# Kernel optimization log

Hardware: AMD Instinct MI355X
Metric: run time of the kernel (lower is better)

The kernel has to match this reference:

```python
import jax, jax.numpy as jnp
import numpy as np

B, S, F = 1024, 256, 64
HD = 64          # hidden_size
MEM = 10         # attention_memory
TIME_IDX = 0


def setup_inputs() -> dict:
    key = jax.random.key(0)
    ks = jax.random.split(key, 20)
    sc = 0.05
    d = {}
    d["x"] = jax.random.normal(ks[0], (B, S, F), dtype=jnp.float32)
    # layer 0 cell: linear_s in = HD+F+1; gates (f,i,T,u,o) stacked: in = HD+F+HD, out = 5*HD
    d["Ws0"] = jax.random.normal(ks[1], (HD + F + 1, HD), dtype=jnp.float32) * sc
    d["bs0"] = jnp.zeros((HD,), dtype=jnp.float32)
    d["Wg0"] = jax.random.normal(ks[2], (HD + F + HD, 5 * HD), dtype=jnp.float32) * sc
    d["bg0"] = jnp.zeros((5 * HD,), dtype=jnp.float32)
    # layer 1 cell: input is h of layer 0 (HD wide)
    d["Ws1"] = jax.random.normal(ks[3], (HD + HD + 1, HD), dtype=jnp.float32) * sc
    d["bs1"] = jnp.zeros((HD,), dtype=jnp.float32)
    d["Wg1"] = jax.random.normal(ks[4], (HD + HD + HD, 5 * HD), dtype=jnp.float32) * sc
    d["bg1"] = jnp.zeros((5 * HD,), dtype=jnp.float32)
    # attention params
    d["Waq"] = jax.random.normal(ks[5], (2 * HD, HD), dtype=jnp.float32) * sc
    d["baq"] = jnp.zeros((HD,), dtype=jnp.float32)
    d["Wah"] = jax.random.normal(ks[6], (HD, HD), dtype=jnp.float32) * sc
    d["bah"] = jnp.zeros((HD,), dtype=jnp.float32)
    d["bias_a"] = jnp.zeros((HD,), dtype=jnp.float32)
    d["v"] = jnp.ones((HD,), dtype=jnp.float32)
    d["Wint"] = jax.random.normal(ks[7], (2 * HD, HD), dtype=jnp.float32) * sc
    d["bint"] = jnp.zeros((HD,), dtype=jnp.float32)
    return d


def _cell(x_t, d_t, h, c, Ws, bs, Wg, bg):
    # s_t = tanh(linear_s([h, x, delta]))
    s = jnp.tanh(jnp.concatenate([h, x_t, d_t], axis=1) @ Ws + bs)
    # fused gate projection: [f, i, T, u(zeta), o] on [h, x, s]
    g = jnp.concatenate([h, x_t, s], axis=1) @ Wg + bg
    f, i, T, u, o = jnp.split(g, 5, axis=1)
    f = jax.nn.sigmoid(f)
    i = jax.nn.sigmoid(i)
    T = jax.nn.sigmoid(T)
    u = jnp.tanh(u)
    o = jax.nn.sigmoid(o)
    c_new = f * c + i * u + T * s
    h_new = o * jnp.tanh(c_new)
    return h_new, c_new


def reference(x, Ws0, bs0, Wg0, bg0, Ws1, bs1, Wg1, bg1,
              Waq, baq, Wah, bah, bias_a, v, Wint, bint):
    b, s_len, _ = x.shape
    hd = bs0.shape[0]
    # delta_t = time[t] - time[t-1], zero at t=0  -> [B, S, 1]
    time = x[:, :, TIME_IDX]
    delta = jnp.concatenate(
        [jnp.zeros((b, 1), dtype=x.dtype), time[:, 1:] - time[:, :-1]], axis=1)[:, :, None]

    xs = jnp.moveaxis(x, 1, 0)       # [S, B, F]
    ds = jnp.moveaxis(delta, 1, 0)   # [S, B, 1]

    def step(carry, inp):
        h0, c0, h1, c1 = carry
        x_t, d_t = inp
        h0, c0 = _cell(x_t, d_t, h0, c0, Ws0, bs0, Wg0, bg0)
        h1, c1 = _cell(h0, d_t, h1, c1, Ws1, bs1, Wg1, bg1)
        return (h0, c0, h1, c1), h1

    z = jnp.zeros((b, hd), dtype=x.dtype)
    (h0, c0, h1, c1), Hseq = jax.lax.scan(step, (z, z, z, z), (xs, ds))
    H = jnp.moveaxis(Hseq, 0, 1)     # [B, S, HD]

    mem = min(s_len, MEM)
    H_mem = H[:, s_len - mem:, :]    # [B, mem, HD]

    q_proj = jnp.concatenate([h1, c1], axis=1) @ Waq + baq   # [B, HD]
    H_proj = H_mem @ Wah + bah                                # [B, mem, HD]
    scores = jnp.tanh(q_proj[:, None, :] + H_proj + bias_a) @ v  # [B, mem]
    alpha = jax.nn.softmax(scores, axis=1)
    e_t = jnp.einsum('bm,bmh->bh', alpha, H_mem)
    final_repr = jnp.tanh(jnp.concatenate([h1, e_t], axis=1) @ Wint + bint)
    return final_repr
```

## Files before the change

kernel.cpp:

```cpp
#include <hip/hip_runtime.h>
#include <math.h>

#define HD    64
#define SLEN  256
#define BATCH 1024
#define TBB   16
#define NB    (BATCH / TBB)
#define NT    256
#define MEMN  10

typedef short bf16x8 __attribute__((ext_vector_type(8)));
typedef float f32x4  __attribute__((ext_vector_type(4)));
typedef unsigned short u16x4 __attribute__((ext_vector_type(4)));

#define MFMA16(a, b, c) __builtin_amdgcn_mfma_f32_16x16x32_bf16((a), (b), (c), 0, 0, 0)

#define OFF_WGL 122880
#define OFF_WSH 245760
#define OFF_WSL 262144
#define OFF_WSR_BYTES 557056

__device__ __forceinline__ unsigned short f2bf(float f) {
  unsigned u = __float_as_uint(f);
  u += 0x7fffu + ((u >> 16) & 1u);
  return (unsigned short)(u >> 16);
}
__device__ __forceinline__ float bf2f(unsigned short h) {
  return __uint_as_float(((unsigned)h) << 16);
}

__device__ __forceinline__ float frcp(float x) {
#if __has_builtin(__builtin_amdgcn_rcpf)
  return __builtin_amdgcn_rcpf(x);
#else
  return 1.0f / x;
#endif
}
__device__ __forceinline__ float fsigm(float v) { return frcp(1.0f + __expf(-v)); }
__device__ __forceinline__ float ftanh(float v) { return 2.0f * frcp(1.0f + __expf(-2.0f * v)) - 1.0f; }

__device__ __forceinline__ void bar_lds() {
  asm volatile("s_waitcnt lgkmcnt(0)" ::: "memory");
  __builtin_amdgcn_s_barrier();
  asm volatile("" ::: "memory");
}

__global__ void __launch_bounds__(256)
prep_pack(const float* __restrict__ Wg0, const float* __restrict__ Wg1,
          const float* __restrict__ Ws0, const float* __restrict__ Ws1,
          unsigned short* __restrict__ ws)
{
  const int idx = blockIdx.x * 256 + threadIdx.x;
  const int NWG = 2 * 20 * 6 * 64 * 8;
  const int NWS = 2 * 4 * 4 * 64 * 8;
  if (idx < NWG) {
    int L = idx / 61440, r0 = idx % 61440;
    int tile = r0 / 3072, r1 = r0 % 3072;
    int ks = r1 / 512, r2 = r1 % 512;
    int lane = r2 / 8, j = r2 % 8;
    int row = ks * 32 + (lane >> 4) * 8 + j;
    int col = tile * 16 + (lane & 15);
    float v = (L ? Wg1 : Wg0)[row * 320 + col];
    unsigned short h = f2bf(v);
    ws[idx] = h;
    ws[OFF_WGL + idx] = f2bf(v - bf2f(h));
  } else if (idx < NWG + NWS) {
    int k = idx - NWG;
    int L = k / 8192, r0 = k % 8192;
    int tile = r0 / 2048, r1 = r0 % 2048;
    int ks = r1 / 512, r2 = r1 % 512;
    int lane = r2 / 8, j = r2 % 8;
    int row = ks * 32 + (lane >> 4) * 8 + j;
    int col = tile * 16 + (lane & 15);
    float v = (L ? Ws1 : Ws0)[row * 64 + col];
    unsigned short h = f2bf(v);
    ws[OFF_WSH + k] = h;
    ws[OFF_WSL + k] = f2bf(v - bf2f(h));
  } else if (idx < NWG + NWS + 128) {
    int k = idx - NWG - NWS;
    int L = k / 64, c = k % 64;
    float* wsr = (float*)((char*)ws + OFF_WSR_BYTES);
    wsr[k] = (L ? Ws1 : Ws0)[128 * 64 + c];
  }
}

struct __align__(16) Smem {
  unsigned short XbH[2][16][216];
  unsigned short XbL[2][16][216];
  unsigned short WgC[2][5][4][2][512];
  float Hm[MEMN][16][64];
  float dlt[2][16];
  float h1s[16][68];
  float c1s[16][68];
};

__global__ void __launch_bounds__(NT, 1)
thlstm_mfma(const float* __restrict__ x, const unsigned short* __restrict__ wpack,
            const float* __restrict__ bs0, const float* __restrict__ bg0,
            const float* __restrict__ bs1, const float* __restrict__ bg1,
            const float* __restrict__ Waq, const float* __restrict__ gbaq,
            const float* __restrict__ Wah, const float* __restrict__ gbah,
            const float* __restrict__ gba,  const float* __restrict__ gv,
            const float* __restrict__ Wint, const float* __restrict__ gbint,
            float* __restrict__ out)
{
  __shared__ Smem sm;
  const int tid = threadIdx.x;
  const int w = tid >> 6, l = tid & 63;
  const int lg = l >> 4, lr = l & 15;
  const int c = w * 16 + lr;
  const int b0 = blockIdx.x * TBB;
  const int xrow = tid >> 4, xq = tid & 15;

  const unsigned short* WgH = wpack;
  const unsigned short* WgL = wpack + OFF_WGL;
  const unsigned short* WsH = wpack + OFF_WSH;
  const unsigned short* WsL = wpack + OFF_WSL;
  const float* WsR = (const float*)((const char*)wpack + OFF_WSR_BYTES);

  for (int i = tid; i < 2 * 16 * 216; i += NT) {
    ((unsigned short*)sm.XbH)[i] = 0;
    ((unsigned short*)sm.XbL)[i] = 0;
  }
  for (int i = tid; i < 5120; i += NT) {
    const int chunk = i & 63, frag = i >> 6;
    const int p = frag & 1, tt = (frag >> 1) & 3;
    const int g = (frag >> 3) % 5, L = (frag >> 3) / 5;
    const unsigned short* src = (p ? WgL : WgH) + ((L * 20 + g * 4 + tt) * 6 + 0) * 512 + chunk * 8;
    *(bf16x8*)&sm.WgC[L][g][tt][p][chunk * 8] = *(const bf16x8*)src;
  }
  if (xq == 0) { sm.dlt[0][xrow] = 0.f; sm.dlt[1][xrow] = 0.f; }

  bf16x8 wsW[2][4][2];
  bf16x8 wgT[2][5][2][2];
#pragma unroll
  for (int L = 0; L < 2; ++L) {
#pragma unroll
    for (int ks = 0; ks < 4; ++ks) {
      const int o = ((L * 4 + w) * 4 + ks) * 512 + l * 8;
      wsW[L][ks][0] = *(const bf16x8*)(WsH + o);
      wsW[L][ks][1] = *(const bf16x8*)(WsL + o);
    }
#pragma unroll
    for (int g = 0; g < 5; ++g)
#pragma unroll
      for (int k2 = 0; k2 < 2; ++k2) {
        const int o = ((L * 20 + g * 4 + w) * 6 + 4 + k2) * 512 + l * 8;
        wgT[L][g][k2][0] = *(const bf16x8*)(WgH + o);
        wgT[L][g][k2][1] = *(const bf16x8*)(WgL + o);
      }
  }
  float bsr[2]  = { bs0[c], bs1[c] };
  float wsrr[2] = { WsR[c], WsR[64 + c] };
  float bgr[2][5];
#pragma unroll
  for (int g = 0; g < 5; ++g) { bgr[0][g] = bg0[g * 64 + c]; bgr[1][g] = bg1[g * 64 + c]; }

  f32x4 xreg = *(const f32x4*)&x[((size_t)(b0 + xrow) * SLEN + 0) * HD + xq * 4];
  float prev0 = xreg[0];
  {
    u16x4 ph, pl;
#pragma unroll
    for (int k = 0; k < 4; ++k) {
      unsigned short hh = f2bf(xreg[k]);
      ph[k] = hh; pl[k] = f2bf(xreg[k] - bf2f(hh));
    }
    *(u16x4*)&sm.XbH[0][xrow][64 + xq * 4] = ph;
    *(u16x4*)&sm.XbL[0][xrow][64 + xq * 4] = pl;
  }
  bar_lds();
  xreg = *(const f32x4*)&x[((size_t)(b0 + xrow) * SLEN + 1) * HD + xq * 4];

  float cst[2][4] = {{0.f,0.f,0.f,0.f},{0.f,0.f,0.f,0.f}};
  float h1v[4] = {0.f,0.f,0.f,0.f};

  bf16x8 w1H[5], w1L[5];
#pragma unroll
  for (int g = 0; g < 5; ++g) {
    const int o1 = ((0 * 20 + g * 4 + w) * 6 + 1) * 512 + l * 8;
    w1H[g] = *(const bf16x8*)(WgH + o1);
    w1L[g] = *(const bf16x8*)(WgL + o1);
  }

  for (int t = 0; t < SLEN; ++t) {
#pragma unroll
    for (int L = 0; L < 2; ++L) {
      bf16x8 w2H[5], w2L[5], w3H[5], w3L[5];
#pragma unroll
      for (int g = 0; g < 5; ++g) {
        const int o2 = ((L * 20 + g * 4 + w) * 6 + 2) * 512 + l * 8;
        const int o3 = ((L * 20 + g * 4 + w) * 6 + 3) * 512 + l * 8;
        w2H[g] = *(const bf16x8*)(WgH + o2);
        w2L[g] = *(const bf16x8*)(WgL + o2);
        w3H[g] = *(const bf16x8*)(WgH + o3);
        w3L[g] = *(const bf16x8*)(WgL + o3);
      }
      bf16x8 aH[4], aL[4];
#pragma unroll
      for (int ks = 0; ks < 4; ++ks) {
        aH[ks] = *(const bf16x8*)&sm.XbH[L][lr][ks * 32 + lg * 8];
        aL[ks] = *(const bf16x8*)&sm.XbL[L][lr][ks * 32 + lg * 8];
      }
      f32x4 sHH = {0.f,0.f,0.f,0.f}, sHL = {0.f,0.f,0.f,0.f}, sLH = {0.f,0.f,0.f,0.f};
#pragma unroll
      for (int ks = 0; ks < 4; ++ks) {
        sHH = MFMA16(aH[ks], wsW[L][ks][0], sHH);
        sHL = MFMA16(aH[ks], wsW[L][ks][1], sHL);
        sLH = MFMA16(aL[ks], wsW[L][ks][0], sLH);
      }
      f32x4 gacc[5];
#pragma unroll
      for (int g = 0; g < 5; ++g) {
        bf16x8 cH = *(const bf16x8*)&sm.WgC[L][g][w][0][l * 8];
        bf16x8 cL = *(const bf16x8*)&sm.WgC[L][g][w][1][l * 8];
        f32x4 acc = {0.f,0.f,0.f,0.f};
        acc = MFMA16(aH[0], cH, acc);
        acc = MFMA16(aH[0], cL, acc);
        acc = MFMA16(aL[0], cH, acc);
        gacc[g] = acc;
      }
#pragma unroll
      for (int g = 0; g < 5; ++g) {
        gacc[g] = MFMA16(aH[1], w1H[g], gacc[g]);
        gacc[g] = MFMA16(aH[1], w1L[g], gacc[g]);
        gacc[g] = MFMA16(aL[1], w1H[g], gacc[g]);
      }
      f32x4 sacc = (sHH + sHL) + sLH;
      float sv[4];
      const float* dltc = sm.dlt[t & 1];
#pragma unroll
      for (int q = 0; q < 4; ++q) {
        const int r = lg * 4 + q;
        sv[q] = ftanh(sacc[q] + bsr[L] + dltc[r] * wsrr[L]);
        unsigned short hh = f2bf(sv[q]);
        sm.XbH[L][r][128 + c] = hh;
        sm.XbL[L][r][128 + c] = f2bf(sv[q] - bf2f(hh));
      }
#pragma unroll
      for (int g = 0; g < 5; ++g) {
        gacc[g] = MFMA16(aH[2], w2H[g], gacc[g]);
        gacc[g] = MFMA16(aH[2], w2L[g], gacc[g]);
        gacc[g] = MFMA16(aL[2], w2H[g], gacc[g]);
      }
      bar_lds();

      bf16x8 sHf[2], sLf[2];
#pragma unroll
      for (int k2 = 0; k2 < 2; ++k2) {
        sHf[k2] = *(const bf16x8*)&sm.XbH[L][lr][128 + k2 * 32 + lg * 8];
        sLf[k2] = *(const bf16x8*)&sm.XbL[L][lr][128 + k2 * 32 + lg * 8];
      }
#pragma unroll
      for (int g = 0; g < 5; ++g) {
        gacc[g] = MFMA16(aH[3], w3H[g], gacc[g]);
        gacc[g] = MFMA16(aH[3], w3L[g], gacc[g]);
        gacc[g] = MFMA16(aL[3], w3H[g], gacc[g]);
      }
#pragma unroll
      for (int k2 = 0; k2 < 2; ++k2)
#pragma unroll
        for (int g = 0; g < 5; ++g) {
          gacc[g] = MFMA16(sHf[k2], wgT[L][g][k2][0], gacc[g]);
          gacc[g] = MFMA16(sHf[k2], wgT[L][g][k2][1], gacc[g]);
          gacc[g] = MFMA16(sLf[k2], wgT[L][g][k2][0], gacc[g]);
        }
      {
        const int nL = 1 - L;
#pragma unroll
        for (int g = 0; g < 5; ++g) {
          const int o1 = ((nL * 20 + g * 4 + w) * 6 + 1) * 512 + l * 8;
          w1H[g] = *(const bf16x8*)(WgH + o1);
          w1L[g] = *(const bf16x8*)(WgL + o1);
        }
      }
#pragma unroll
      for (int q = 0; q < 4; ++q) {
        const int r = lg * 4 + q;
        const float fg = fsigm(gacc[0][q] + bgr[L][0]);
        const float ig = fsigm(gacc[1][q] + bgr[L][1]);
        const float Tg = fsigm(gacc[2][q] + bgr[L][2]);
        const float ug = ftanh(gacc[3][q] + bgr[L][3]);
        const float og = fsigm(gacc[4][q] + bgr[L][4]);
        const float cn = fg * cst[L][q] + ig * ug + Tg * sv[q];
        cst[L][q] = cn;
        const float hn = og * ftanh(cn);
        const unsigned short hh = f2bf(hn), hl = f2bf(hn - bf2f(hh));
        if (L == 0) {
          sm.XbH[0][r][c] = hh;      sm.XbL[0][r][c] = hl;
          sm.XbH[1][r][64 + c] = hh; sm.XbL[1][r][64 + c] = hl;
        } else {
          sm.XbH[1][r][c] = hh;      sm.XbL[1][r][c] = hl;
          h1v[q] = hn;
          if (t >= SLEN - MEMN) sm.Hm[t - (SLEN - MEMN)][r][c] = hn;
        }
      }
      if (L == 0) {
        if (xq == 0) { sm.dlt[(t + 1) & 1][xrow] = xreg[0] - prev0; prev0 = xreg[0]; }
        u16x4 ph, pl;
#pragma unroll
        for (int k = 0; k < 4; ++k) {
          unsigned short hh = f2bf(xreg[k]);
          ph[k] = hh; pl[k] = f2bf(xreg[k] - bf2f(hh));
        }
        *(u16x4*)&sm.XbH[0][xrow][64 + xq * 4] = ph;
        *(u16x4*)&sm.XbL[0][xrow][64 + xq * 4] = pl;
        const int tn = (t + 2 < SLEN) ? (t + 2) : (SLEN - 1);
        xreg = *(const f32x4*)&x[((size_t)(b0 + xrow) * SLEN + tn) * HD + xq * 4];
      }
      bar_lds();
    }
  }

#pragma unroll
  for (int q = 0; q < 4; ++q) {
    const int r = lg * 4 + q;
    sm.h1s[r][c] = h1v[q];
    sm.c1s[r][c] = cst[1][q];
  }
  bar_lds();

  float evs[4];
#pragma unroll
  for (int ri = 0; ri < 4; ++ri) {
    const int r = 4 * w + ri;
    const int j = l;
    float qv = gbaq[j];
    for (int k = 0; k < 64; ++k) qv += sm.h1s[r][k] * Waq[k * 64 + j];
    for (int k = 0; k < 64; ++k) qv += sm.c1s[r][k] * Waq[(64 + k) * 64 + j];
    float sc[MEMN];
#pragma unroll
    for (int m = 0; m < MEMN; ++m) {
      float hp = gbah[j];
      for (int k = 0; k < 64; ++k) hp += sm.Hm[m][r][k] * Wah[k * 64 + j];
      float tv = tanhf(qv + hp + gba[j]) * gv[j];
#pragma unroll
      for (int off = 32; off; off >>= 1) tv += __shfl_xor(tv, off, 64);
      sc[m] = tv;
    }
    float mx = sc[0];
#pragma unroll
    for (int m = 1; m < MEMN; ++m) mx = fmaxf(mx, sc[m]);
    float den = 0.f;
#pragma unroll
    for (int m = 0; m < MEMN; ++m) { sc[m] = expf(sc[m] - mx); den += sc[m]; }
    const float inv = 1.f / den;
    float ev = 0.f;
#pragma unroll
    for (int m = 0; m < MEMN; ++m) ev += sc[m] * sm.Hm[m][r][j];
    evs[ri] = ev * inv;
  }
  float (*es)[68] = sm.c1s;
#pragma unroll
  for (int ri = 0; ri < 4; ++ri) es[4 * w + ri][l] = evs[ri];
  bar_lds();
#pragma unroll
  for (int ri = 0; ri < 4; ++ri) {
    const int r = 4 * w + ri;
    const int j = l;
    float acc = gbint[j];
    for (int k = 0; k < 64; ++k) acc += sm.h1s[r][k] * Wint[k * 64 + j];
    for (int k = 0; k < 64; ++k) acc += es[r][k] * Wint[(64 + k) * 64 + j];
    out[(size_t)(b0 + r) * HD + j] = tanhf(acc);
  }
}

extern "C" void kernel_launch(void* const* d_in, const int* in_sizes, int n_in,
                              void* d_out, int out_size, void* d_ws, size_t ws_size,
                              hipStream_t stream) {
  const float* x      = (const float*)d_in[0];
  const float* Ws0    = (const float*)d_in[1];
  const float* bs0    = (const float*)d_in[2];
  const float* Wg0    = (const float*)d_in[3];
  const float* bg0    = (const float*)d_in[4];
  const float* Ws1    = (const float*)d_in[5];
  const float* bs1    = (const float*)d_in[6];
  const float* Wg1    = (const float*)d_in[7];
  const float* bg1    = (const float*)d_in[8];
  const float* Waq    = (const float*)d_in[9];
  const float* baq    = (const float*)d_in[10];
  const float* Wah    = (const float*)d_in[11];
  const float* bah    = (const float*)d_in[12];
  const float* bias_a = (const float*)d_in[13];
  const float* v      = (const float*)d_in[14];
  const float* Wint   = (const float*)d_in[15];
  const float* bint   = (const float*)d_in[16];
  float* out = (float*)d_out;

  const int total = 2 * 20 * 6 * 64 * 8 + 2 * 4 * 4 * 64 * 8 + 128;
  prep_pack<<<(total + 255) / 256, 256, 0, stream>>>(Wg0, Wg1, Ws0, Ws1,
                                                     (unsigned short*)d_ws);
  thlstm_mfma<<<NB, NT, 0, stream>>>(x, (const unsigned short*)d_ws,
                                     bs0, bg0, bs1, bg1,
                                     Waq, baq, Wah, bah, bias_a, v, Wint, bint, out);
}
```

Baseline: 1.279 ms.

## Skew two LSTM layers into wavefront so both run per tick

Restructures the recurrence so that each tick computes layer 0 at time t and layer 1 at time t-1 together, with a prologue for layer 0 at t=0 and an epilogue for layer 1 at the last step. This halves the number of barrier-separated phases per timestep and exposes two independent MFMA chains to interleave, hiding latency. In exchange, register pressure roughly doubles (two sets of weight fragments and accumulators), which may lower occupancy or cause spills, and the code grows.

```diff
diff --git a/kernel.cpp b/kernel.cpp
--- a/kernel.cpp
+++ b/kernel.cpp
@@ -8,6 +8,7 @@
 #define NB    (BATCH / TBB)
 #define NT    256
 #define MEMN  10
+#define LASTT (SLEN - MEMN)
 
 typedef short bf16x8 __attribute__((ext_vector_type(8)));
 typedef float f32x4  __attribute__((ext_vector_type(4)));
@@ -174,140 +175,385 @@
   float cst[2][4] = {{0.f,0.f,0.f,0.f},{0.f,0.f,0.f,0.f}};
   float h1v[4] = {0.f,0.f,0.f,0.f};
 
-  bf16x8 w1H[5], w1L[5];
-#pragma unroll
-  for (int g = 0; g < 5; ++g) {
-    const int o1 = ((0 * 20 + g * 4 + w) * 6 + 1) * 512 + l * 8;
-    w1H[g] = *(const bf16x8*)(WgH + o1);
-    w1L[g] = *(const bf16x8*)(WgL + o1);
-  }
-
-  for (int t = 0; t < SLEN; ++t) {
-#pragma unroll
-    for (int L = 0; L < 2; ++L) {
-      bf16x8 w2H[5], w2L[5], w3H[5], w3L[5];
-#pragma unroll
-      for (int g = 0; g < 5; ++g) {
-        const int o2 = ((L * 20 + g * 4 + w) * 6 + 2) * 512 + l * 8;
-        const int o3 = ((L * 20 + g * 4 + w) * 6 + 3) * 512 + l * 8;
-        w2H[g] = *(const bf16x8*)(WgH + o2);
-        w2L[g] = *(const bf16x8*)(WgL + o2);
-        w3H[g] = *(const bf16x8*)(WgH + o3);
-        w3L[g] = *(const bf16x8*)(WgL + o3);
-      }
-      bf16x8 aH[4], aL[4];
+  {
+    bf16x8 w1H[5], w1L[5];
+#pragma unroll
+    for (int g = 0; g < 5; ++g) {
+      const int o1 = ((g * 4 + w) * 6 + 1) * 512 + l * 8;
+      w1H[g] = *(const bf16x8*)(WgH + o1);
+      w1L[g] = *(const bf16x8*)(WgL + o1);
+    }
+    bf16x8 aH[4], aL[4];
+#pragma unroll
+    for (int ks = 0; ks < 4; ++ks) {
+      aH[ks] = *(const bf16x8*)&sm.XbH[0][lr][ks * 32 + lg * 8];
+      aL[ks] = *(const bf16x8*)&sm.XbL[0][lr][ks * 32 + lg * 8];
+    }
+    f32x4 sHH = {0,0,0,0}, sHL = {0,0,0,0}, sLH = {0,0,0,0};
+#pragma unroll
+    for (int ks = 0; ks < 4; ++ks) {
+      sHH = MFMA16(aH[ks], wsW[0][ks][0], sHH);
+      sHL = MFMA16(aH[ks], wsW[0][ks][1], sHL);
+      sLH = MFMA16(aL[ks], wsW[0][ks][0], sLH);
+    }
+    f32x4 gacc[5];
+#pragma unroll
+    for (int g = 0; g < 5; ++g) {
+      bf16x8 cH = *(const bf16x8*)&sm.WgC[0][g][w][0][l * 8];
+      bf16x8 cL = *(const bf16x8*)&sm.WgC[0][g][w][1][l * 8];
+      f32x4 acc = {0,0,0,0};
+      acc = MFMA16(aH[0], cH, acc);
+      acc = MFMA16(aH[0], cL, acc);
+      acc = MFMA16(aL[0], cH, acc);
+      gacc[g] = acc;
+    }
+    bf16x8 w2H[5], w2L[5];
+#pragma unroll
+    for (int g = 0; g < 5; ++g) {
+      const int o2 = ((g * 4 + w) * 6 + 2) * 512 + l * 8;
+      w2H[g] = *(const bf16x8*)(WgH + o2);
+      w2L[g] = *(const bf16x8*)(WgL + o2);
+      gacc[g] = MFMA16(aH[1], w1H[g], gacc[g]);
+      gacc[g] = MFMA16(aH[1], w1L[g], gacc[g]);
+      gacc[g] = MFMA16(aL[1], w1H[g], gacc[g]);
+    }
+    f32x4 sacc = (sHH + sHL) + sLH;
+    float sv[4];
+#pragma unroll
+    for (int q = 0; q < 4; ++q) {
+      const int r = lg * 4 + q;
+      sv[q] = ftanh(sacc[q] + bsr[0]);
+      unsigned short hh = f2bf(sv[q]);
+      sm.XbH[0][r][128 + c] = hh;
+      sm.XbL[0][r][128 + c] = f2bf(sv[q] - bf2f(hh));
+    }
+#pragma unroll
+    for (int g = 0; g < 5; ++g) {
+      gacc[g] = MFMA16(aH[2], w2H[g], gacc[g]);
+      gacc[g] = MFMA16(aH[2], w2L[g], gacc[g]);
+      gacc[g] = MFMA16(aL[2], w2H[g], gacc[g]);
+    }
+    bar_lds();
+    bf16x8 w3H[5], w3L[5];
+#pragma unroll
+    for (int g = 0; g < 5; ++g) {
+      const int o3 = ((g * 4 + w) * 6 + 3) * 512 + l * 8;
+      w3H[g] = *(const bf16x8*)(WgH + o3);
+      w3L[g] = *(const bf16x8*)(WgL + o3);
+    }
+    bf16x8 sHf[2], sLf[2];
+#pragma unroll
+    for (int k2 = 0; k2 < 2; ++k2) {
+      sHf[k2] = *(const bf16x8*)&sm.XbH[0][lr][128 + k2 * 32 + lg * 8];
+      sLf[k2] = *(const bf16x8*)&sm.XbL[0][lr][128 + k2 * 32 + lg * 8];
+    }
+#pragma unroll
+    for (int k2 = 0; k2 < 2; ++k2)
+#pragma unroll
+      for (int g = 0; g < 5; ++g) {
+        gacc[g] = MFMA16(sHf[k2], wgT[0][g][k2][0], gacc[g]);
+        gacc[g] = MFMA16(sHf[k2], wgT[0][g][k2][1], gacc[g]);
+        gacc[g] = MFMA16(sLf[k2], wgT[0][g][k2][0], gacc[g]);
+      }
+#pragma unroll
+    for (int g = 0; g < 5; ++g) {
+      gacc[g] = MFMA16(aH[3], w3H[g], gacc[g]);
+      gacc[g] = MFMA16(aH[3], w3L[g], gacc[g]);
+      gacc[g] = MFMA16(aL[3], w3H[g], gacc[g]);
+    }
+#pragma unroll
+    for (int q = 0; q < 4; ++q) {
+      const int r = lg * 4 + q;
+      const float fg = fsigm(gacc[0][q] + bgr[0][0]);
+      const float ig = fsigm(gacc[1][q] + bgr[0][1]);
+      const float Tg = fsigm(gacc[2][q] + bgr[0][2]);
+      const float ug = ftanh(gacc[3][q] + bgr[0][3]);
+      const float og = fsigm(gacc[4][q] + bgr[0][4]);
+      const float cn = fg * cst[0][q] + ig * ug + Tg * sv[q];
+      cst[0][q] = cn;
+      const float hn = og * ftanh(cn);
+      const unsigned short hh = f2bf(hn), hl = f2bf(hn - bf2f(hh));
+      sm.XbH[0][r][c] = hh;      sm.XbL[0][r][c] = hl;
+      sm.XbH[1][r][64 + c] = hh; sm.XbL[1][r][64 + c] = hl;
+    }
+    if (xq == 0) { sm.dlt[1][xrow] = xreg[0] - prev0; prev0 = xreg[0]; }
+    {
+      u16x4 ph, pl;
+#pragma unroll
+      for (int k = 0; k < 4; ++k) {
+        unsigned short hh = f2bf(xreg[k]);
+        ph[k] = hh; pl[k] = f2bf(xreg[k] - bf2f(hh));
+      }
+      *(u16x4*)&sm.XbH[0][xrow][64 + xq * 4] = ph;
+      *(u16x4*)&sm.XbL[0][xrow][64 + xq * 4] = pl;
+    }
+    xreg = *(const f32x4*)&x[((size_t)(b0 + xrow) * SLEN + 2) * HD + xq * 4];
+    bar_lds();
+  }
+
+  for (int tick = 1; tick < SLEN; ++tick) {
+    bf16x8 w1H[2][5], w1L[2][5];
+#pragma unroll
+    for (int Lc = 0; Lc < 2; ++Lc)
+#pragma unroll
+      for (int g = 0; g < 5; ++g) {
+        const int o1 = ((Lc * 20 + g * 4 + w) * 6 + 1) * 512 + l * 8;
+        w1H[Lc][g] = *(const bf16x8*)(WgH + o1);
+        w1L[Lc][g] = *(const bf16x8*)(WgL + o1);
+      }
+    bf16x8 aH[2][4], aL[2][4];
+#pragma unroll
+    for (int Lc = 0; Lc < 2; ++Lc)
 #pragma unroll
       for (int ks = 0; ks < 4; ++ks) {
-        aH[ks] = *(const bf16x8*)&sm.XbH[L][lr][ks * 32 + lg * 8];
-        aL[ks] = *(const bf16x8*)&sm.XbL[L][lr][ks * 32 + lg * 8];
-      }
-      f32x4 sHH = {0.f,0.f,0.f,0.f}, sHL = {0.f,0.f,0.f,0.f}, sLH = {0.f,0.f,0.f,0.f};
+        aH[Lc][ks] = *(const bf16x8*)&sm.XbH[Lc][lr][ks * 32 + lg * 8];
+        aL[Lc][ks] = *(const bf16x8*)&sm.XbL[Lc][lr][ks * 32 + lg * 8];
+      }
+    f32x4 sHH[2], sHL[2], sLH[2];
+#pragma unroll
+    for (int Lc = 0; Lc < 2; ++Lc) {
+      sHH[Lc] = (f32x4){0,0,0,0}; sHL[Lc] = (f32x4){0,0,0,0}; sLH[Lc] = (f32x4){0,0,0,0};
 #pragma unroll
       for (int ks = 0; ks < 4; ++ks) {
-        sHH = MFMA16(aH[ks], wsW[L][ks][0], sHH);
-        sHL = MFMA16(aH[ks], wsW[L][ks][1], sHL);
-        sLH = MFMA16(aL[ks], wsW[L][ks][0], sLH);
-      }
-      f32x4 gacc[5];
-#pragma unroll
-      for (int g = 0; g < 5; ++g) {
-        bf16x8 cH = *(const bf16x8*)&sm.WgC[L][g][w][0][l * 8];
-        bf16x8 cL = *(const bf16x8*)&sm.WgC[L][g][w][1][l * 8];
-        f32x4 acc = {0.f,0.f,0.f,0.f};
-        acc = MFMA16(aH[0], cH, acc);
-        acc = MFMA16(aH[0], cL, acc);
-        acc = MFMA16(aL[0], cH, acc);
-        gacc[g] = acc;
-      }
-#pragma unroll
-      for (int g = 0; g < 5; ++g) {
-        gacc[g] = MFMA16(aH[1], w1H[g], gacc[g]);
-        gacc[g] = MFMA16(aH[1], w1L[g], gacc[g]);
-        gacc[g] = MFMA16(aL[1], w1H[g], gacc[g]);
-      }
-      f32x4 sacc = (sHH + sHL) + sLH;
-      float sv[4];
-      const float* dltc = sm.dlt[t & 1];
+        sHH[Lc] = MFMA16(aH[Lc][ks], wsW[Lc][ks][0], sHH[Lc]);
+        sHL[Lc] = MFMA16(aH[Lc][ks], wsW[Lc][ks][1], sHL[Lc]);
+        sLH[Lc] = MFMA16(aL[Lc][ks], wsW[Lc][ks][0], sLH[Lc]);
+      }
+    }
+    f32x4 gacc[2][5];
+#pragma unroll
+    for (int Lc = 0; Lc < 2; ++Lc)
+#pragma unroll
+      for (int g = 0; g < 5; ++g) {
+        bf16x8 cH = *(const bf16x8*)&sm.WgC[Lc][g][w][0][l * 8];
+        bf16x8 cL = *(const bf16x8*)&sm.WgC[Lc][g][w][1][l * 8];
+        f32x4 acc = {0,0,0,0};
+        acc = MFMA16(aH[Lc][0], cH, acc);
+        acc = MFMA16(aH[Lc][0], cL, acc);
+        acc = MFMA16(aL[Lc][0], cH, acc);
+        gacc[Lc][g] = acc;
+      }
+    bf16x8 w2H[2][5], w2L[2][5];
+#pragma unroll
+    for (int Lc = 0; Lc < 2; ++Lc)
+#pragma unroll
+      for (int g = 0; g < 5; ++g) {
+        const int o2 = ((Lc * 20 + g * 4 + w) * 6 + 2) * 512 + l * 8;
+        w2H[Lc][g] = *(const bf16x8*)(WgH + o2);
+        w2L[Lc][g] = *(const bf16x8*)(WgL + o2);
+        gacc[Lc][g] = MFMA16(aH[Lc][1], w1H[Lc][g], gacc[Lc][g]);
+        gacc[Lc][g] = MFMA16(aH[Lc][1], w1L[Lc][g], gacc[Lc][g]);
+        gacc[Lc][g] = MFMA16(aL[Lc][1], w1H[Lc][g], gacc[Lc][g]);
+      }
+    float sv[2][4];
+    const float* dltA = sm.dlt[tick & 1];
+    const float* dltB = sm.dlt[(tick & 1) ^ 1];
+#pragma unroll
+    for (int Lc = 0; Lc < 2; ++Lc) {
+      const float* dltc = Lc ? dltB : dltA;
+      f32x4 sacc = (sHH[Lc] + sHL[Lc]) + sLH[Lc];
 #pragma unroll
       for (int q = 0; q < 4; ++q) {
         const int r = lg * 4 + q;
-        sv[q] = ftanh(sacc[q] + bsr[L] + dltc[r] * wsrr[L]);
-        unsigned short hh = f2bf(sv[q]);
-        sm.XbH[L][r][128 + c] = hh;
-        sm.XbL[L][r][128 + c] = f2bf(sv[q] - bf2f(hh));
-      }
-#pragma unroll
-      for (int g = 0; g < 5; ++g) {
-        gacc[g] = MFMA16(aH[2], w2H[g], gacc[g]);
-        gacc[g] = MFMA16(aH[2], w2L[g], gacc[g]);
-        gacc[g] = MFMA16(aL[2], w2H[g], gacc[g]);
-      }
-      bar_lds();
-
-      bf16x8 sHf[2], sLf[2];
+        sv[Lc][q] = ftanh(sacc[q] + bsr[Lc] + dltc[r] * wsrr[Lc]);
+        unsigned short hh = f2bf(sv[Lc][q]);
+        sm.XbH[Lc][r][128 + c] = hh;
+        sm.XbL[Lc][r][128 + c] = f2bf(sv[Lc][q] - bf2f(hh));
+      }
+    }
+#pragma unroll
+    for (int Lc = 0; Lc < 2; ++Lc)
+#pragma unroll
+      for (int g = 0; g < 5; ++g) {
+        gacc[Lc][g] = MFMA16(aH[Lc][2], w2H[Lc][g], gacc[Lc][g]);
+        gacc[Lc][g] = MFMA16(aH[Lc][2], w2L[Lc][g], gacc[Lc][g]);
+        gacc[Lc][g] = MFMA16(aL[Lc][2], w2H[Lc][g], gacc[Lc][g]);
+      }
+    bar_lds();
+
+    bf16x8 w3H[2][5], w3L[2][5];
+#pragma unroll
+    for (int Lc = 0; Lc < 2; ++Lc)
+#pragma unroll
+      for (int g = 0; g < 5; ++g) {
+        const int o3 = ((Lc * 20 + g * 4 + w) * 6 + 3) * 512 + l * 8;
+        w3H[Lc][g] = *(const bf16x8*)(WgH + o3);
+        w3L[Lc][g] = *(const bf16x8*)(WgL + o3);
+      }
+    bf16x8 sHf[2][2], sLf[2][2];
+#pragma unroll
+    for (int Lc = 0; Lc < 2; ++Lc)
 #pragma unroll
       for (int k2 = 0; k2 < 2; ++k2) {
-        sHf[k2] = *(const bf16x8*)&sm.XbH[L][lr][128 + k2 * 32 + lg * 8];
-        sLf[k2] = *(const bf16x8*)&sm.XbL[L][lr][128 + k2 * 32 + lg * 8];
-      }
-#pragma unroll
-      for (int g = 0; g < 5; ++g) {
-        gacc[g] = MFMA16(aH[3], w3H[g], gacc[g]);
-        gacc[g] = MFMA16(aH[3], w3L[g], gacc[g]);
-        gacc[g] = MFMA16(aL[3], w3H[g], gacc[g]);
-      }
+        sHf[Lc][k2] = *(const bf16x8*)&sm.XbH[Lc][lr][128 + k2 * 32 + lg * 8];
+        sLf[Lc][k2] = *(const bf16x8*)&sm.XbL[Lc][lr][128 + k2 * 32 + lg * 8];
+      }
+#pragma unroll
+    for (int Lc = 0; Lc < 2; ++Lc)
 #pragma unroll
       for (int k2 = 0; k2 < 2; ++k2)
 #pragma unroll
         for (int g = 0; g < 5; ++g) {
-          gacc[g] = MFMA16(sHf[k2], wgT[L][g][k2][0], gacc[g]);
-          gacc[g] = MFMA16(sHf[k2], wgT[L][g][k2][1], gacc[g]);
-          gacc[g] = MFMA16(sLf[k2], wgT[L][g][k2][0], gacc[g]);
+          gacc[Lc][g] = MFMA16(sHf[Lc][k2], wgT[Lc][g][k2][0], gacc[Lc][g]);
+          gacc[Lc][g] = MFMA16(sHf[Lc][k2], wgT[Lc][g][k2][1], gacc[Lc][g]);
+          gacc[Lc][g] = MFMA16(sLf[Lc][k2], wgT[Lc][g][k2][0], gacc[Lc][g]);
         }
+#pragma unroll
+    for (int Lc = 0; Lc < 2; ++Lc)
+#pragma unroll
+      for (int g = 0; g < 5; ++g) {
+        gacc[Lc][g] = MFMA16(aH[Lc][3], w3H[Lc][g], gacc[Lc][g]);
+        gacc[Lc][g] = MFMA16(aH[Lc][3], w3L[Lc][g], gacc[Lc][g]);
+        gacc[Lc][g] = MFMA16(aL[Lc][3], w3H[Lc][g], gacc[Lc][g]);
+      }
+#pragma unroll
+    for (int q = 0; q < 4; ++q) {
+      const int r = lg * 4 + q;
       {
-        const int nL = 1 - L;
-#pragma unroll
-        for (int g = 0; g < 5; ++g) {
-          const int o1 = ((nL * 20 + g * 4 + w) * 6 + 1) * 512 + l * 8;
-          w1H[g] = *(const bf16x8*)(WgH + o1);
-          w1L[g] = *(const bf16x8*)(WgL + o1);
-        }
-      }
-#pragma unroll
-      for (int q = 0; q < 4; ++q) {
-        const int r = lg * 4 + q;
-        const float fg = fsigm(gacc[0][q] + bgr[L][0]);
-        const float ig = fsigm(gacc[1][q] + bgr[L][1]);
-        const float Tg = fsigm(gacc[2][q] + bgr[L][2]);
-        const float ug = ftanh(gacc[3][q] + bgr[L][3]);
-        const float og = fsigm(gacc[4][q] + bgr[L][4]);
-        const float cn = fg * cst[L][q] + ig * ug + Tg * sv[q];
-        cst[L][q] = cn;
+        const float fg = fsigm(gacc[0][0][q] + bgr[0][0]);
+        const float ig = fsigm(gacc[0][1][q] + bgr[0][1]);
+        const float Tg = fsigm(gacc[0][2][q] + bgr[0][2]);
+        const float ug = ftanh(gacc[0][3][q] + bgr[0][3]);
+        const float og = fsigm(gacc[0][4][q] + bgr[0][4]);
+        const float cn = fg * cst[0][q] + ig * ug + Tg * sv[0][q];
+        cst[0][q] = cn;
         const float hn = og * ftanh(cn);
         const unsigned short hh = f2bf(hn), hl = f2bf(hn - bf2f(hh));
-        if (L == 0) {
-          sm.XbH[0][r][c] = hh;      sm.XbL[0][r][c] = hl;
-          sm.XbH[1][r][64 + c] = hh; sm.XbL[1][r][64 + c] = hl;
-        } else {
-          sm.XbH[1][r][c] = hh;      sm.XbL[1][r][c] = hl;
-          h1v[q] = hn;
-          if (t >= SLEN - MEMN) sm.Hm[t - (SLEN - MEMN)][r][c] = hn;
-        }
-      }
-      if (L == 0) {
-        if (xq == 0) { sm.dlt[(t + 1) & 1][xrow] = xreg[0] - prev0; prev0 = xreg[0]; }
-        u16x4 ph, pl;
-#pragma unroll
-        for (int k = 0; k < 4; ++k) {
-          unsigned short hh = f2bf(xreg[k]);
-          ph[k] = hh; pl[k] = f2bf(xreg[k] - bf2f(hh));
-        }
-        *(u16x4*)&sm.XbH[0][xrow][64 + xq * 4] = ph;
-        *(u16x4*)&sm.XbL[0][xrow][64 + xq * 4] = pl;
-        const int tn = (t + 2 < SLEN) ? (t + 2) : (SLEN - 1);
-        xreg = *(const f32x4*)&x[((size_t)(b0 + xrow) * SLEN + tn) * HD + xq * 4];
-      }
-      bar_lds();
+        sm.XbH[0][r][c] = hh;      sm.XbL[0][r][c] = hl;
+        sm.XbH[1][r][64 + c] = hh; sm.XbL[1][r][64 + c] = hl;
+      }
+      {
+        const float fg = fsigm(gacc[1][0][q] + bgr[1][0]);
+        const float ig = fsigm(gacc[1][1][q] + bgr[1][1]);
+        const float Tg = fsigm(gacc[1][2][q] + bgr[1][2]);
+        const float ug = ftanh(gacc[1][3][q] + bgr[1][3]);
+        const float og = fsigm(gacc[1][4][q] + bgr[1][4]);
+        const float cn = fg * cst[1][q] + ig * ug + Tg * sv[1][q];
+        cst[1][q] = cn;
+        const float hn = og * ftanh(cn);
+        const unsigned short hh = f2bf(hn), hl = f2bf(hn - bf2f(hh));
+        sm.XbH[1][r][c] = hh;      sm.XbL[1][r][c] = hl;
+        if (tick - 1 >= LASTT) sm.Hm[tick - 1 - LASTT][r][c] = hn;
+      }
+    }
+    if (xq == 0) { sm.dlt[(tick + 1) & 1][xrow] = xreg[0] - prev0; prev0 = xreg[0]; }
+    {
+      u16x4 ph, pl;
+#pragma unroll
+      for (int k = 0; k < 4; ++k) {
+        unsigned short hh = f2bf(xreg[k]);
+        ph[k] = hh; pl[k] = f2bf(xreg[k] - bf2f(hh));
+      }
+      *(u16x4*)&sm.XbH[0][xrow][64 + xq * 4] = ph;
+      *(u16x4*)&sm.XbL[0][xrow][64 + xq * 4] = pl;
+    }
+    {
+      const int tn = (tick + 2 < SLEN) ? (tick + 2) : (SLEN - 1);
+      xreg = *(const f32x4*)&x[((size_t)(b0 + xrow) * SLEN + tn) * HD + xq * 4];
+    }
+    bar_lds();
+  }
+
+  {
+    bf16x8 w1H[5], w1L[5];
+#pragma unroll
+    for (int g = 0; g < 5; ++g) {
+      const int o1 = ((20 + g * 4 + w) * 6 + 1) * 512 + l * 8;
+      w1H[g] = *(const bf16x8*)(WgH + o1);
+      w1L[g] = *(const bf16x8*)(WgL + o1);
+    }
+    bf16x8 aH[4], aL[4];
+#pragma unroll
+    for (int ks = 0; ks < 4; ++ks) {
+      aH[ks] = *(const bf16x8*)&sm.XbH[1][lr][ks * 32 + lg * 8];
+      aL[ks] = *(const bf16x8*)&sm.XbL[1][lr][ks * 32 + lg * 8];
+    }
+    f32x4 sHH = {0,0,0,0}, sHL = {0,0,0,0}, sLH = {0,0,0,0};
+#pragma unroll
+    for (int ks = 0; ks < 4; ++ks) {
+      sHH = MFMA16(aH[ks], wsW[1][ks][0], sHH);
+      sHL = MFMA16(aH[ks], wsW[1][ks][1], sHL);
+      sLH = MFMA16(aL[ks], wsW[1][ks][0], sLH);
+    }
+    f32x4 gacc[5];
+#pragma unroll
+    for (int g = 0; g < 5; ++g) {
+      bf16x8 cH = *(const bf16x8*)&sm.WgC[1][g][w][0][l * 8];
+      bf16x8 cL = *(const bf16x8*)&sm.WgC[1][g][w][1][l * 8];
+      f32x4 acc = {0,0,0,0};
+      acc = MFMA16(aH[0], cH, acc);
+      acc = MFMA16(aH[0], cL, acc);
+      acc = MFMA16(aL[0], cH, acc);
+      gacc[g] = acc;
+    }
+    bf16x8 w2H[5], w2L[5];
+#pragma unroll
+    for (int g = 0; g < 5; ++g) {
+      const int o2 = ((20 + g * 4 + w) * 6 + 2) * 512 + l * 8;
+      w2H[g] = *(const bf16x8*)(WgH + o2);
+      w2L[g] = *(const bf16x8*)(WgL + o2);
+      gacc[g] = MFMA16(aH[1], w1H[g], gacc[g]);
+      gacc[g] = MFMA16(aH[1], w1L[g], gacc[g]);
+      gacc[g] = MFMA16(aL[1], w1H[g], gacc[g]);
+    }
+    f32x4 sacc = (sHH + sHL) + sLH;
+    float sv[4];
+    const float* dltc = sm.dlt[(SLEN - 1) & 1];
+#pragma unroll
+    for (int q = 0; q < 4; ++q) {
+      const int r = lg * 4 + q;
+      sv[q] = ftanh(sacc[q] + bsr[1] + dltc[r] * wsrr[1]);
+      unsigned short hh = f2bf(sv[q]);
+      sm.XbH[1][r][128 + c] = hh;
+      sm.XbL[1][r][128 + c] = f2bf(sv[q] - bf2f(hh));
+    }
+#pragma unroll
+    for (int g = 0; g < 5; ++g) {
+      gacc[g] = MFMA16(aH[2], w2H[g], gacc[g]);
+      gacc[g] = MFMA16(aH[2], w2L[g], gacc[g]);
+      gacc[g] = MFMA16(aL[2], w2H[g], gacc[g]);
+    }
+    bar_lds();
+    bf16x8 w3H[5], w3L[5];
+#pragma unroll
+    for (int g = 0; g < 5; ++g) {
+      const int o3 = ((20 + g * 4 + w) * 6 + 3) * 512 + l * 8;
+      w3H[g] = *(const bf16x8*)(WgH + o3);
+      w3L[g] = *(const bf16x8*)(WgL + o3);
+    }
+    bf16x8 sHf[2], sLf[2];
+#pragma unroll
+    for (int k2 = 0; k2 < 2; ++k2) {
+      sHf[k2] = *(const bf16x8*)&sm.XbH[1][lr][128 + k2 * 32 + lg * 8];
+      sLf[k2] = *(const bf16x8*)&sm.XbL[1][lr][128 + k2 * 32 + lg * 8];
+    }
+#pragma unroll
+    for (int k2 = 0; k2 < 2; ++k2)
+#pragma unroll
+      for (int g = 0; g < 5; ++g) {
+        gacc[g] = MFMA16(sHf[k2], wgT[1][g][k2][0], gacc[g]);
+        gacc[g] = MFMA16(sHf[k2], wgT[1][g][k2][1], gacc[g]);
+        gacc[g] = MFMA16(sLf[k2], wgT[1][g][k2][0], gacc[g]);
+      }
+#pragma unroll
+    for (int g = 0; g < 5; ++g) {
+      gacc[g] = MFMA16(aH[3], w3H[g], gacc[g]);
+      gacc[g] = MFMA16(aH[3], w3L[g], gacc[g]);
+      gacc[g] = MFMA16(aL[3], w3H[g], gacc[g]);
+    }
+#pragma unroll
+    for (int q = 0; q < 4; ++q) {
+      const int r = lg * 4 + q;
+      const float fg = fsigm(gacc[0][q] + bgr[1][0]);
+      const float ig = fsigm(gacc[1][q] + bgr[1][1]);
+      const float Tg = fsigm(gacc[2][q] + bgr[1][2]);
+      const float ug = ftanh(gacc[3][q] + bgr[1][3]);
+      const float og = fsigm(gacc[4][q] + bgr[1][4]);
+      const float cn = fg * cst[1][q] + ig * ug + Tg * sv[q];
+      cst[1][q] = cn;
+      const float hn = og * ftanh(cn);
+      h1v[q] = hn;
+      sm.Hm[MEMN - 1][r][c] = hn;
     }
   }
 
```

Measured after the change: 1.930 ms. +50.9%, slower.
